# Kernel optimization log

Hardware: AMD Instinct MI355X
Metric: run time of the kernel (lower is better)

Reference implementation:

```python
import jax, jax.numpy as jnp
import numpy as np

Q_OFFSET = 128  # stored quants are in [0,255); subtract to get signed int8 range


def setup_inputs() -> dict:
    key = jax.random.key(0)
    k1, k2, k3, k4 = jax.random.split(key, 4)
    O, NB, BS = 4096, 128, 32  # out_features, num_blocks, block_size (Q8_0)
    x = jax.random.normal(k1, (4, 1024, NB * BS), dtype=jnp.float16)
    q_weight = jax.random.randint(k2, (O, NB, BS), 0, 255, dtype=jnp.int32)
    scales = jax.random.uniform(k3, (O, NB), dtype=jnp.float16) * jnp.float16(0.05)
    bias = jax.random.normal(k4, (O,), dtype=jnp.float16)
    return {"x": x, "q_weight": q_weight, "scales": scales, "bias": bias}


def reference(x, q_weight, scales, bias):
    # GGUF Q8_0-style on-the-fly dequant: w[o, b*32+j] = (q[o,b,j]-128) * scale[o,b]
    q = q_weight.astype(jnp.float16) - jnp.float16(Q_OFFSET)  # [O, NB, BS]
    w = (q * scales[:, :, None]).reshape(scales.shape[0], -1)  # [O, I]
    # linear: y = x @ w^T + bias
    return jnp.einsum('bsi,oi->bso', x, w) + bias
```

## Files before the change

### kernel.cpp

```cpp
#include <hip/hip_runtime.h>
#include <stdint.h>


#define QOFF 128

typedef __bf16 bf16_t;
typedef __bf16 bf16x8 __attribute__((ext_vector_type(8)));
typedef float f32x4 __attribute__((ext_vector_type(4)));

#define W_VM4 0x0F74
#define W_VM0 0x0F70

__global__ __launch_bounds__(256) void prep_kernel(
    const int* __restrict__ q, const float* __restrict__ scales,
    const float* __restrict__ X, bf16_t* __restrict__ W,
    bf16_t* __restrict__ Xb, int K, int NB, int nDeq) {
  const int b = blockIdx.x;
  if (b < nDeq) {
    const size_t e = ((size_t)b * 256 + threadIdx.x) * 8;
    const int o = (int)(e / (size_t)K);
    const int i = (int)(e % (size_t)K);
    const float s = scales[o * NB + (i >> 5)];
    int4 a = *(const int4*)(q + e);
    int4 c = *(const int4*)(q + e + 4);
    const int* av = (const int*)&a;
    const int* cv = (const int*)&c;
    bf16x8 t;
#pragma unroll
    for (int j = 0; j < 4; ++j) t[j] = (bf16_t)((float)(av[j] - QOFF) * s);
#pragma unroll
    for (int j = 0; j < 4; ++j) t[4 + j] = (bf16_t)((float)(cv[j] - QOFF) * s);
    *(bf16x8*)(W + e) = t;
  } else {
    const size_t e = ((size_t)(b - nDeq) * 256 + threadIdx.x) * 8;
    float4 a = *(const float4*)(X + e);
    float4 c = *(const float4*)(X + e + 4);
    bf16x8 t;
    t[0] = (bf16_t)a.x; t[1] = (bf16_t)a.y; t[2] = (bf16_t)a.z; t[3] = (bf16_t)a.w;
    t[4] = (bf16_t)c.x; t[5] = (bf16_t)c.y; t[6] = (bf16_t)c.z; t[7] = (bf16_t)c.w;
    *(bf16x8*)(Xb + e) = t;
  }
}

__device__ __forceinline__ void async16(bf16_t* lds, const bf16_t* g) {
  __builtin_amdgcn_global_load_lds(
      (const __attribute__((address_space(1))) unsigned int*)(const void*)g,
      (__attribute__((address_space(3))) unsigned int*)(void*)lds, 16, 0, 0);
}

template <int QM, int QN>
__device__ __forceinline__ void mm_block(f32x4 (&acc)[8][4],
                                         const bf16x8 (&af)[4][2],
                                         const bf16x8 (&bv)[2][2]) {
  __builtin_amdgcn_s_setprio(1);
#pragma unroll
  for (int ks = 0; ks < 2; ++ks)
#pragma unroll
    for (int fi = 0; fi < 4; ++fi)
#pragma unroll
      for (int fj = 0; fj < 2; ++fj)
        acc[QM * 4 + fi][QN * 2 + fj] = __builtin_amdgcn_mfma_f32_16x16x32_bf16(
            af[fi][ks], bv[fj][ks], acc[QM * 4 + fi][QN * 2 + fj], 0, 0, 0);
  __builtin_amdgcn_s_setprio(0);
}

__device__ __forceinline__ void rd_a(const bf16_t* base, const int* swz,
                                     bf16x8 (&af)[4][2]) {
#pragma unroll
  for (int ks = 0; ks < 2; ++ks)
#pragma unroll
    for (int fi = 0; fi < 4; ++fi)
      af[fi][ks] = *(const bf16x8*)(base + fi * 1024 + swz[ks]);
}

__device__ __forceinline__ void rd_b(const bf16_t* base, const int* swz,
                                     bf16x8 (&bv)[2][2]) {
#pragma unroll
  for (int ks = 0; ks < 2; ++ks)
#pragma unroll
    for (int fj = 0; fj < 2; ++fj)
      bv[fj][ks] = *(const bf16x8*)(base + fj * 1024 + swz[ks]);
}

__device__ __forceinline__ void rd12(const bf16_t* abase, const bf16_t* bbase,
                                     const int* swz, bf16x8 (&af)[4][2],
                                     bf16x8 (&bv)[2][2]) {
#pragma unroll
  for (int ks = 0; ks < 2; ++ks) {
    af[0][ks] = *(const bf16x8*)(abase + swz[ks]);
    bv[0][ks] = *(const bf16x8*)(bbase + swz[ks]);
    af[1][ks] = *(const bf16x8*)(abase + 1024 + swz[ks]);
    bv[1][ks] = *(const bf16x8*)(bbase + 1024 + swz[ks]);
    af[2][ks] = *(const bf16x8*)(abase + 2048 + swz[ks]);
    af[3][ks] = *(const bf16x8*)(abase + 3072 + swz[ks]);
  }
}

__global__ __launch_bounds__(512, 2) void gemm_8ph(
    const bf16_t* __restrict__ A,
    const bf16_t* __restrict__ B,
    const float* __restrict__ bias,
    float* __restrict__ C,
    int M, int N, int K) {
  __shared__ bf16_t lsA[2][256 * 64];
  __shared__ bf16_t lsB[2][256 * 64];

  const int tid = threadIdx.x;
  const int lane = tid & 63;
  const int wave = tid >> 6;
  const int r = lane & 15;
  const int qd = lane >> 4;
  const int wm = (wave >> 2) * 128;
  const int wn = (wave & 3) * 64;

  const int nbx = N >> 8;
  const int nwg = gridDim.x;
  int wg = blockIdx.x;
  if ((nwg & 7) == 0) wg = (wg & 7) * (nwg >> 3) + (wg >> 3);
  const int m0 = (wg / nbx) * 256;
  const int n0 = (wg % nbx) * 256;

  f32x4 acc[8][4] = {};

  const int srow = tid >> 3;
  const int sslot = (tid & 7) ^ (srow & 7);
  const bf16_t* gA0 = A + (size_t)(m0 + srow) * K + sslot * 8;
  const bf16_t* gB0 = B + (size_t)(n0 + srow) * K + sslot * 8;

  auto stgA = [&](bf16_t* dstTile, int half, int koff) {
    bf16_t* d = dstTile + half * 8192 + tid * 8;
    const bf16_t* g = gA0 + (size_t)(half * 128) * K + koff;
    async16(d, g);
    async16(d + 4096, g + 64 * (size_t)K);
  };
  auto stgB = [&](bf16_t* dstTile, int half, int koff) {
    bf16_t* d = dstTile + half * 8192 + tid * 8;
    const bf16_t* g = gB0 + (size_t)(half * 128) * K + koff;
    async16(d, g);
    async16(d + 4096, g + 64 * (size_t)K);
  };

  const int swz[2] = {(qd ^ (r & 7)) * 8, ((4 + qd) ^ (r & 7)) * 8};
  const bf16_t* a0base = &lsA[0][(wm + r) * 64];
  const bf16_t* a1base = &lsA[1][(wm + r) * 64];
  const bf16_t* b0base = &lsB[0][(wn + r) * 64];
  const bf16_t* b1base = &lsB[1][(wn + r) * 64];

  const int NT = K >> 6;
  const int NITER = NT >> 1;

  stgA(lsA[0], 0, 0);
  stgA(lsA[0], 1, 0);
  stgB(lsB[0], 0, 0);
  stgB(lsB[0], 1, 0);
  stgB(lsB[1], 0, 64);
  stgB(lsB[1], 1, 64);
  __builtin_amdgcn_s_waitcnt(W_VM4);
  __builtin_amdgcn_s_barrier();

  bf16x8 af[4][2], bf0[2][2], bf1[2][2];

#pragma unroll 1
  for (int j = 0; j < NITER; ++j) {
    const int k1 = (2 * j + 1) * 64;
    int t2 = 2 * j + 2; if (t2 >= NT) t2 -= NT;
    int t3 = 2 * j + 3; if (t3 >= NT) t3 -= NT;
    const int k2 = t2 * 64;
    const int k3 = t3 * 64;

    rd12(a0base, b0base, swz, af, bf0);
    stgA(lsA[1], 0, k1);
    mm_block<0, 0>(acc, af, bf0);
    __builtin_amdgcn_s_barrier();
    rd_b(b0base + 2048, swz, bf1);
    stgA(lsA[1], 1, k1);
    mm_block<0, 1>(acc, af, bf1);
    __builtin_amdgcn_s_barrier();
    rd_a(a0base + 4096, swz, af);
    stgB(lsB[0], 0, k2);
    mm_block<1, 1>(acc, af, bf1);
    __builtin_amdgcn_s_barrier();
    stgB(lsB[0], 1, k2);
    mm_block<1, 0>(acc, af, bf0);
    __builtin_amdgcn_s_waitcnt(W_VM4);
    __builtin_amdgcn_s_barrier();

    rd12(a1base, b1base, swz, af, bf0);
    stgA(lsA[0], 0, k2);
    mm_block<0, 0>(acc, af, bf0);
    __builtin_amdgcn_s_barrier();
    rd_b(b1base + 2048, swz, bf1);
    stgA(lsA[0], 1, k2);
    mm_block<0, 1>(acc, af, bf1);
    __builtin_amdgcn_s_barrier();
    rd_a(a1base + 4096, swz, af);
    stgB(lsB[1], 0, k3);
    mm_block<1, 1>(acc, af, bf1);
    __builtin_amdgcn_s_barrier();
    stgB(lsB[1], 1, k3);
    mm_block<1, 0>(acc, af, bf0);
    __builtin_amdgcn_s_waitcnt(W_VM4);
    __builtin_amdgcn_s_barrier();
  }

  __builtin_amdgcn_s_waitcnt(W_VM0);

#pragma unroll
  for (int ni = 0; ni < 4; ++ni) {
    const int n = n0 + wn + ni * 16 + r;
    const float bv = bias[n];
#pragma unroll
    for (int mi = 0; mi < 8; ++mi) {
      const int mbase = m0 + wm + mi * 16 + qd * 4;
#pragma unroll
      for (int reg = 0; reg < 4; ++reg) {
        C[(size_t)(mbase + reg) * N + n] = acc[mi][ni][reg] + bv;
      }
    }
  }
}

__global__ __launch_bounds__(256) void gemm_db(
    const bf16_t* __restrict__ A, const bf16_t* __restrict__ B,
    const float* __restrict__ bias, float* __restrict__ C, int M, int N,
    int K) {
  __shared__ bf16_t lsA[2][128 * 32];
  __shared__ bf16_t lsB[2][128 * 32];

  const int tid = threadIdx.x;
  const int lane = tid & 63;
  const int wave = tid >> 6;
  const int m0 = blockIdx.y * 128;
  const int n0 = blockIdx.x * 128;
  const int wm = (wave >> 1) * 64;
  const int wn = (wave & 1) * 64;
  const int r = lane & 15;
  const int qd = lane >> 4;

  f32x4 acc[4][4] = {};

  const int e0 = tid * 8;
  const int e1 = 2048 + tid * 8;
  const bf16_t* gA0 = A + (size_t)(m0 + (e0 >> 5)) * K + (e0 & 31);
  const bf16_t* gA1 = A + (size_t)(m0 + (e1 >> 5)) * K + (e1 & 31);
  const bf16_t* gB0 = B + (size_t)(n0 + (e0 >> 5)) * K + (e0 & 31);
  const bf16_t* gB1 = B + (size_t)(n0 + (e1 >> 5)) * K + (e1 & 31);

  async16(&lsA[0][e0], gA0);
  async16(&lsA[0][e1], gA1);
  async16(&lsB[0][e0], gB0);
  async16(&lsB[0][e1], gB1);

  int buf = 0;
  for (int k0 = 0; k0 < K; k0 += 32, buf ^= 1) {
    __syncthreads();
    if (k0 + 32 < K) {
      const int nk = k0 + 32;
      async16(&lsA[buf ^ 1][e0], gA0 + nk);
      async16(&lsA[buf ^ 1][e1], gA1 + nk);
      async16(&lsB[buf ^ 1][e0], gB0 + nk);
      async16(&lsB[buf ^ 1][e1], gB1 + nk);
    }
    bf16x8 af[4], bfv[4];
#pragma unroll
    for (int i = 0; i < 4; ++i) {
      af[i] = *(const bf16x8*)&lsA[buf][(wm + i * 16 + r) * 32 + qd * 8];
      bfv[i] = *(const bf16x8*)&lsB[buf][(wn + i * 16 + r) * 32 + qd * 8];
    }
#pragma unroll
    for (int mi = 0; mi < 4; ++mi)
#pragma unroll
      for (int ni = 0; ni < 4; ++ni)
        acc[mi][ni] = __builtin_amdgcn_mfma_f32_16x16x32_bf16(
            af[mi], bfv[ni], acc[mi][ni], 0, 0, 0);
  }

#pragma unroll
  for (int ni = 0; ni < 4; ++ni) {
    const int n = n0 + wn + ni * 16 + r;
    const float bv = bias[n];
#pragma unroll
    for (int mi = 0; mi < 4; ++mi) {
      const int mbase = m0 + wm + mi * 16 + qd * 4;
#pragma unroll
      for (int reg = 0; reg < 4; ++reg) {
        C[(size_t)(mbase + reg) * N + n] = acc[mi][ni][reg] + bv;
      }
    }
  }
}

__global__ __launch_bounds__(256) void gemm_fused(
    const float* __restrict__ Af, const int* __restrict__ q,
    const float* __restrict__ scales, const float* __restrict__ bias,
    float* __restrict__ C, int M, int N, int K, int NB) {
  __shared__ bf16_t lsA[128 * 32];
  __shared__ bf16_t lsB[128 * 32];

  const int tid = threadIdx.x;
  const int lane = tid & 63;
  const int wave = tid >> 6;
  const int m0 = blockIdx.y * 128;
  const int n0 = blockIdx.x * 128;
  const int wm = (wave >> 1) * 64;
  const int wn = (wave & 1) * 64;
  const int r = lane & 15;
  const int qd = lane >> 4;

  const int e = tid * 16;
  const int row = e >> 5;
  const int col = e & 31;

  const float* gAf = Af + (size_t)(m0 + row) * K + col;
  const int* gQ = q + (size_t)(n0 + row) * K + col;
  const float* gS = scales + (size_t)(n0 + row) * NB;

  f32x4 acc[4][4] = {};

  for (int k0 = 0; k0 < K; k0 += 32) {
    bf16x8 a0, a1, b0, b1;
    {
      float4 f0 = *(const float4*)(gAf + k0);
      float4 f1 = *(const float4*)(gAf + k0 + 4);
      float4 f2 = *(const float4*)(gAf + k0 + 8);
      float4 f3 = *(const float4*)(gAf + k0 + 12);
      a0[0] = (bf16_t)f0.x; a0[1] = (bf16_t)f0.y; a0[2] = (bf16_t)f0.z; a0[3] = (bf16_t)f0.w;
      a0[4] = (bf16_t)f1.x; a0[5] = (bf16_t)f1.y; a0[6] = (bf16_t)f1.z; a0[7] = (bf16_t)f1.w;
      a1[0] = (bf16_t)f2.x; a1[1] = (bf16_t)f2.y; a1[2] = (bf16_t)f2.z; a1[3] = (bf16_t)f2.w;
      a1[4] = (bf16_t)f3.x; a1[5] = (bf16_t)f3.y; a1[6] = (bf16_t)f3.z; a1[7] = (bf16_t)f3.w;
    }
    {
      const float s = gS[k0 >> 5];
      int qv[16];
      *(int4*)&qv[0] = *(const int4*)(gQ + k0);
      *(int4*)&qv[4] = *(const int4*)(gQ + k0 + 4);
      *(int4*)&qv[8] = *(const int4*)(gQ + k0 + 8);
      *(int4*)&qv[12] = *(const int4*)(gQ + k0 + 12);
#pragma unroll
      for (int j = 0; j < 8; ++j) b0[j] = (bf16_t)((float)(qv[j] - QOFF) * s);
#pragma unroll
      for (int j = 0; j < 8; ++j)
        b1[j] = (bf16_t)((float)(qv[8 + j] - QOFF) * s);
    }

    __syncthreads();
    *(bf16x8*)&lsA[e] = a0;
    *(bf16x8*)&lsA[e + 8] = a1;
    *(bf16x8*)&lsB[e] = b0;
    *(bf16x8*)&lsB[e + 8] = b1;
    __syncthreads();

    bf16x8 af[4], bfv[4];
#pragma unroll
    for (int i = 0; i < 4; ++i) {
      af[i] = *(const bf16x8*)&lsA[(wm + i * 16 + r) * 32 + qd * 8];
      bfv[i] = *(const bf16x8*)&lsB[(wn + i * 16 + r) * 32 + qd * 8];
    }
#pragma unroll
    for (int mi = 0; mi < 4; ++mi)
#pragma unroll
      for (int ni = 0; ni < 4; ++ni)
        acc[mi][ni] = __builtin_amdgcn_mfma_f32_16x16x32_bf16(
            af[mi], bfv[ni], acc[mi][ni], 0, 0, 0);
  }

#pragma unroll
  for (int ni = 0; ni < 4; ++ni) {
    const int n = n0 + wn + ni * 16 + r;
    const float bv = bias[n];
#pragma unroll
    for (int mi = 0; mi < 4; ++mi) {
      const int mbase = m0 + wm + mi * 16 + qd * 4;
#pragma unroll
      for (int reg = 0; reg < 4; ++reg) {
        C[(size_t)(mbase + reg) * N + n] = acc[mi][ni][reg] + bv;
      }
    }
  }
}

extern "C" void kernel_launch(void* const* d_in, const int* in_sizes, int n_in,
                              void* d_out, int out_size, void* d_ws,
                              size_t ws_size, hipStream_t stream) {
  const float* x = (const float*)d_in[0];
  const int* qw = (const int*)d_in[1];
  const float* scales = (const float*)d_in[2];
  const float* bias = (const float*)d_in[3];
  float* out = (float*)d_out;

  const int O = in_sizes[3];
  const int K = in_sizes[1] / O;
  const int NB = in_sizes[2] / O;
  const int M = in_sizes[0] / K;
  (void)n_in; (void)out_size;

  const size_t Wbytes = (size_t)O * K * sizeof(bf16_t);
  const size_t Xbytes = (size_t)M * K * sizeof(bf16_t);

  if (ws_size >= Wbytes + Xbytes) {
    bf16_t* W = (bf16_t*)d_ws;
    bf16_t* Xb = (bf16_t*)((char*)d_ws + Wbytes);
    const int nDeq = (int)((size_t)O * K / 2048);
    const int nCvt = (int)((size_t)M * K / 2048);
    prep_kernel<<<nDeq + nCvt, 256, 0, stream>>>(qw, scales, x, W, Xb, K, NB,
                                                 nDeq);
    if ((M % 256) == 0 && (O % 256) == 0 && (K % 128) == 0) {
      const int nwg = (M / 256) * (O / 256);
      gemm_8ph<<<nwg, 512, 0, stream>>>(Xb, W, bias, out, M, O, K);
    } else {
      dim3 grid(O / 128, M / 128);
      gemm_db<<<grid, 256, 0, stream>>>(Xb, W, bias, out, M, O, K);
    }
  } else {
    dim3 grid(O / 128, M / 128);
    gemm_fused<<<grid, 256, 0, stream>>>(x, qw, scales, bias, out, M, O, K,
                                         NB);
  }
}
```

Measured before the change: 292.5 us.

## Restructure GEMM main loop to prefetch next tile fragments across stages

After: 287.3 us. No clear change (-1.8%).

```diff
diff --git a/kernel.cpp b/kernel.cpp
--- a/kernel.cpp
+++ b/kernel.cpp
@@ -147,61 +147,53 @@
   const bf16_t* b1base = &lsB[1][(wn + r) * 64];
 
   const int NT = K >> 6;
-  const int NITER = NT >> 1;
+
+  bf16x8 af_lo[4][2], af_hi[4][2], bv0[2][2], bv1[2][2];
 
   stgA(lsA[0], 0, 0);
   stgA(lsA[0], 1, 0);
   stgB(lsB[0], 0, 0);
   stgB(lsB[0], 1, 0);
+  stgA(lsA[1], 0, 64);
+  stgA(lsA[1], 1, 64);
+  __builtin_amdgcn_s_waitcnt(W_VM4);
+  __builtin_amdgcn_s_barrier();
+  rd12(a0base, b0base, swz, af_lo, bv0);
   stgB(lsB[1], 0, 64);
   stgB(lsB[1], 1, 64);
-  __builtin_amdgcn_s_waitcnt(W_VM4);
+
+#define TILE_STEP(CUR, NXT, K2)                                       \
+                                                              \
+  mm_block<0, 0>(acc, af_lo, bv0);                                    \
+  rd_a(a##CUR##base + 4096, swz, af_hi);                              \
+  __builtin_amdgcn_s_barrier();                                       \
+                                                              \
+  mm_block<1, 0>(acc, af_hi, bv0);                                    \
+  rd_b(b##CUR##base + 2048, swz, bv1);                                \
+  __builtin_amdgcn_s_barrier();                                       \
+                                                              \
+  mm_block<0, 1>(acc, af_lo, bv1);                                    \
+  stgA(lsA[CUR], 0, K2);                                              \
+  stgA(lsA[CUR], 1, K2);                                              \
+  __builtin_amdgcn_s_waitcnt(W_VM4);                                  \
+  __builtin_amdgcn_s_barrier();                                       \
+                                                              \
+  mm_block<1, 1>(acc, af_hi, bv1);                                    \
+  rd12(a##NXT##base, b##NXT##base, swz, af_lo, bv0);                  \
+  stgB(lsB[CUR], 0, K2);                                              \
+  stgB(lsB[CUR], 1, K2);                                              \
   __builtin_amdgcn_s_barrier();
 
-  bf16x8 af[4][2], bf0[2][2], bf1[2][2];
-
 #pragma unroll 1
-  for (int j = 0; j < NITER; ++j) {
-    const int k1 = (2 * j + 1) * 64;
+  for (int j = 0; j < NT / 2; ++j) {
     int t2 = 2 * j + 2; if (t2 >= NT) t2 -= NT;
     int t3 = 2 * j + 3; if (t3 >= NT) t3 -= NT;
     const int k2 = t2 * 64;
     const int k3 = t3 * 64;
-
-    rd12(a0base, b0base, swz, af, bf0);
-    stgA(lsA[1], 0, k1);
-    mm_block<0, 0>(acc, af, bf0);
-    __builtin_amdgcn_s_barrier();
-    rd_b(b0base + 2048, swz, bf1);
-    stgA(lsA[1], 1, k1);
-    mm_block<0, 1>(acc, af, bf1);
-    __builtin_amdgcn_s_barrier();
-    rd_a(a0base + 4096, swz, af);
-    stgB(lsB[0], 0, k2);
-    mm_block<1, 1>(acc, af, bf1);
-    __builtin_amdgcn_s_barrier();
-    stgB(lsB[0], 1, k2);
-    mm_block<1, 0>(acc, af, bf0);
-    __builtin_amdgcn_s_waitcnt(W_VM4);
-    __builtin_amdgcn_s_barrier();
-
-    rd12(a1base, b1base, swz, af, bf0);
-    stgA(lsA[0], 0, k2);
-    mm_block<0, 0>(acc, af, bf0);
-    __builtin_amdgcn_s_barrier();
-    rd_b(b1base + 2048, swz, bf1);
-    stgA(lsA[0], 1, k2);
-    mm_block<0, 1>(acc, af, bf1);
-    __builtin_amdgcn_s_barrier();
-    rd_a(a1base + 4096, swz, af);
-    stgB(lsB[1], 0, k3);
-    mm_block<1, 1>(acc, af, bf1);
-    __builtin_amdgcn_s_barrier();
-    stgB(lsB[1], 1, k3);
-    mm_block<1, 0>(acc, af, bf0);
-    __builtin_amdgcn_s_waitcnt(W_VM4);
-    __builtin_amdgcn_s_barrier();
-  }
+    TILE_STEP(0, 1, k2)
+    TILE_STEP(1, 0, k3)
+  }
+#undef TILE_STEP
 
   __builtin_amdgcn_s_waitcnt(W_VM0);
 
```
